# Kernel optimization log

Hardware: AMD Instinct MI355X
Metric: run time of the kernel (lower is better)

## Reference

```python
import jax, jax.numpy as jnp
import numpy as np

B, S, D, H = 4, 1024, 2048, 16
HD = D // H
SCALE = float(np.sqrt(HD))


def setup_inputs() -> dict:
    key = jax.random.key(0)
    ks = jax.random.split(key, 11)
    std = 1.0 / np.sqrt(D)
    inp = {
        'q': jax.random.normal(ks[0], (B, S, D), jnp.float32),
        'k': jax.random.normal(ks[1], (B, S, D), jnp.float32),
        'v': jax.random.normal(ks[2], (B, S, D), jnp.float32),
        'wq_w': jax.random.uniform(ks[3], (D, D), jnp.float32, -std, std),
        'wq_b': jax.random.uniform(ks[4], (D,), jnp.float32, -std, std),
        'wk_w': jax.random.uniform(ks[5], (D, D), jnp.float32, -std, std),
        'wk_b': jax.random.uniform(ks[6], (D,), jnp.float32, -std, std),
        'wv_w': jax.random.uniform(ks[7], (D, D), jnp.float32, -std, std),
        'wv_b': jax.random.uniform(ks[8], (D,), jnp.float32, -std, std),
        'wo_w': jax.random.uniform(ks[9], (D, D), jnp.float32, -std, std),
        'wo_b': jax.random.uniform(ks[10], (D,), jnp.float32, -std, std),
    }
    return inp


def reference(q, k, v, wq_w, wq_b, wk_w, wk_b, wv_w, wv_b, wo_w, wo_b):
    # Linear projections (torch Linear: x @ W.T + b), split into heads: [B,H,S,HD]
    Q = (q @ wq_w.T + wq_b).reshape(B, S, H, HD).transpose(0, 2, 1, 3)
    K = (k @ wk_w.T + wk_b).reshape(B, S, H, HD).transpose(0, 2, 1, 3)
    V = (v @ wv_w.T + wv_b).reshape(B, S, H, HD).transpose(0, 2, 1, 3)
    # scaled dot-product attention; mask=None, dropout identity (eval)
    scores = jnp.einsum('bhqd,bhkd->bhqk', Q, K) / SCALE  # [B,H,S,S]
    attn = jax.nn.softmax(scores, axis=-1)
    context = jnp.einsum('bhqk,bhkd->bhqd', attn, V)      # [B,H,S,HD]
    context = context.transpose(0, 2, 1, 3).reshape(B, S, D)
    output = context @ wo_w.T + wo_b
    return output, attn
```

## Files before the change

kernel.cpp:

```cpp
#include <hip/hip_runtime.h>
#include <hip/hip_bf16.h>


typedef __attribute__((ext_vector_type(4)))  float f32x4;
typedef __attribute__((ext_vector_type(16))) float f32x16;
typedef __attribute__((ext_vector_type(8))) short  bf16x8;
typedef __attribute__((ext_vector_type(4))) short  short4v;
typedef __attribute__((ext_vector_type(8))) short  short8v;

__device__ __forceinline__ short f2b(float f) {
  __hip_bfloat16 h = __float2bfloat16(f);
  return __builtin_bit_cast(short, h);
}
__device__ __forceinline__ float b2f(short s) {
  __hip_bfloat16 h = __builtin_bit_cast(__hip_bfloat16, s);
  return __bfloat162float(h);
}

__global__ void cast_all(
    const float* __restrict__ q,  const float* __restrict__ k,  const float* __restrict__ v,
    const float* __restrict__ w0, const float* __restrict__ w1, const float* __restrict__ w2,
    const float* __restrict__ w3,
    __hip_bfloat16* __restrict__ qd, __hip_bfloat16* __restrict__ kd, __hip_bfloat16* __restrict__ vd,
    __hip_bfloat16* __restrict__ d0, __hip_bfloat16* __restrict__ d1, __hip_bfloat16* __restrict__ d2,
    __hip_bfloat16* __restrict__ d3)
{
  const int c0 = blockIdx.x * blockDim.x + threadIdx.x;
#pragma unroll
  for (int it = 0; it < 10; ++it) {
    int c = c0 + it * 524288;
    const float* in; __hip_bfloat16* out; size_t off;
    if (c < 3145728) {
      int seg = c >> 20; off = (size_t)(c & 1048575) * 8;
      in  = seg == 0 ? q  : (seg == 1 ? k  : v);
      out = seg == 0 ? qd : (seg == 1 ? kd : vd);
    } else {
      int c2 = c - 3145728;
      int seg = c2 >> 19; off = (size_t)(c2 & 524287) * 8;
      in  = seg == 0 ? w0 : (seg == 1 ? w1 : (seg == 2 ? w2 : w3));
      out = seg == 0 ? d0 : (seg == 1 ? d1 : (seg == 2 ? d2 : d3));
    }
    float4 a = *(const float4*)(in + off);
    float4 b = *(const float4*)(in + off + 4);
    short8v o;
    o[0] = f2b(a.x); o[1] = f2b(a.y); o[2] = f2b(a.z); o[3] = f2b(a.w);
    o[4] = f2b(b.x); o[5] = f2b(b.y); o[6] = f2b(b.z); o[7] = f2b(b.w);
    *(short8v*)(out + off) = o;
  }
}

__device__ __forceinline__ void gload_lds16(const __hip_bfloat16* g, char* l) {
  __builtin_amdgcn_global_load_lds(
      (const __attribute__((address_space(1))) unsigned int*)g,
      (__attribute__((address_space(3))) unsigned int*)l, 16, 0, 0);
}

template<bool SWAP>
__device__ __forceinline__ void gemm_core64(
    const __hip_bfloat16* ga0, const __hip_bfloat16* gb0,
    char* As, char* Bs, char* lA0, char* lB0,
    int wm, int wn, int l16, int g, f32x4 (&acc)[4][4])
{
  const int sw = (l16 & 7) << 4;
#pragma unroll 1
  for (int kt = 0; kt < 32; ++kt) {
    __syncthreads();
#pragma unroll
    for (int c = 0; c < 4; ++c) {
      gload_lds16(ga0 + c * 16384, lA0 + c * 1024);
      gload_lds16(gb0 + c * 16384, lB0 + c * 1024);
    }
    ga0 += 64; gb0 += 64;
    asm volatile("s_waitcnt vmcnt(0)" ::: "memory");
    __syncthreads();
#pragma unroll
    for (int ks = 0; ks < 2; ++ks) {
      bf16x8 a[4];
#pragma unroll
      for (int mf = 0; mf < 4; ++mf)
        a[mf] = *(const bf16x8*)(As + (wm + mf * 16 + l16) * 128 + ((ks * 64 + g * 16) ^ sw));
#pragma unroll
      for (int nf = 0; nf < 4; ++nf) {
        bf16x8 b = *(const bf16x8*)(Bs + (wn + nf * 16 + l16) * 128 + ((ks * 64 + g * 16) ^ sw));
#pragma unroll
        for (int mf = 0; mf < 4; ++mf) {
          if (SWAP)
            acc[mf][nf] = __builtin_amdgcn_mfma_f32_16x16x32_bf16(b, a[mf], acc[mf][nf], 0, 0, 0);
          else
            acc[mf][nf] = __builtin_amdgcn_mfma_f32_16x16x32_bf16(a[mf], b, acc[mf][nf], 0, 0, 0);
        }
      }
    }
  }
}

__device__ __forceinline__ const __hip_bfloat16* stage_src(
    const __hip_bfloat16* M, int base, int wid, int lane) {
  return M + (size_t)(base + wid * 32 + (lane >> 3)) * 2048
           + (((lane & 7) ^ ((lane >> 3) & 7)) * 8);
}

__global__ __launch_bounds__(256, 3) void gemm_qkv(
    const __hip_bfloat16* __restrict__ qbf, const __hip_bfloat16* __restrict__ kbf,
    const __hip_bfloat16* __restrict__ vbf,
    const __hip_bfloat16* __restrict__ wqb, const __hip_bfloat16* __restrict__ wkb,
    const __hip_bfloat16* __restrict__ wvb,
    const float* __restrict__ bq, const float* __restrict__ bk, const float* __restrict__ bv,
    __hip_bfloat16* __restrict__ Qh, __hip_bfloat16* __restrict__ Kh,
    __hip_bfloat16* __restrict__ Vt)
{
  __shared__ __align__(16) char smem[32768];
  char* As = smem;
  char* Bs = smem + 16384;

  const int z = blockIdx.z;
  const __hip_bfloat16* A  = z == 0 ? qbf : (z == 1 ? kbf : vbf);
  const __hip_bfloat16* Bt = z == 0 ? wqb : (z == 1 ? wkb : wvb);
  const float* bias        = z == 0 ? bq  : (z == 1 ? bk  : bv);
  __hip_bfloat16* C        = z == 0 ? Qh  : (z == 1 ? Kh  : Vt);

  const int tid  = threadIdx.x;
  const int lane = tid & 63, wid = tid >> 6;
  const int l16  = lane & 15, g = lane >> 4;
  const int m0 = blockIdx.y * 128, n0 = blockIdx.x * 128;
  const int wm = (wid >> 1) * 64, wn = (wid & 1) * 64;

  f32x4 acc[4][4];
#pragma unroll
  for (int i = 0; i < 4; ++i)
#pragma unroll
    for (int j = 0; j < 4; ++j) acc[i][j] = f32x4{0.f, 0.f, 0.f, 0.f};

  const __hip_bfloat16* ga0 = stage_src(A,  m0, wid, lane);
  const __hip_bfloat16* gb0 = stage_src(Bt, n0, wid, lane);
  char* lA0 = As + wid * 4096;
  char* lB0 = Bs + wid * 4096;

  if (z == 2) gemm_core64<false>(ga0, gb0, As, Bs, lA0, lB0, wm, wn, l16, g, acc);
  else        gemm_core64<true >(ga0, gb0, As, Bs, lA0, lB0, wm, wn, l16, g, acc);

  const int hh = n0 >> 7, bb = m0 >> 10, sbase = m0 & 1023;
  const int c8 = (tid & 15) * 8;
  char* Cs = smem;
  if (z != 2) {
#pragma unroll
    for (int h = 0; h < 2; ++h) {
      __syncthreads();
      if ((wid >> 1) == h) {
#pragma unroll
        for (int nf = 0; nf < 4; ++nf) {
          f32x4 bvv = *(const f32x4*)(bias + n0 + wn + nf * 16 + g * 4);
#pragma unroll
          for (int mf = 0; mf < 4; ++mf) {
            int sl = mf * 16 + l16;
            int hd = wn + nf * 16 + g * 4;
            short4v pk;
#pragma unroll
            for (int r = 0; r < 4; ++r) pk[r] = f2b(acc[mf][nf][r] + bvv[r]);
            *(short4v*)(Cs + sl * 272 + hd * 2) = pk;
          }
        }
      }
      __syncthreads();
#pragma unroll
      for (int p = 0; p < 4; ++p) {
        int rl = p * 16 + (tid >> 4);
        bf16x8 val = *(const bf16x8*)(Cs + rl * 272 + c8 * 2);
        *(bf16x8*)(C + (((size_t)bb * 16 + hh) * 1024 + sbase + h * 64 + rl) * 128 + c8) = val;
      }
    }
  } else {
#pragma unroll
    for (int h = 0; h < 2; ++h) {
      __syncthreads();
      if ((wid & 1) == h) {
#pragma unroll
        for (int nf = 0; nf < 4; ++nf) {
          float bvv = bias[n0 + wn + nf * 16 + l16];
#pragma unroll
          for (int mf = 0; mf < 4; ++mf) {
            int hdl = nf * 16 + l16;
            int s0  = wm + mf * 16 + g * 4;
            short4v pk;
#pragma unroll
            for (int r = 0; r < 4; ++r) pk[r] = f2b(acc[mf][nf][r] + bvv);
            *(short4v*)(Cs + hdl * 272 + s0 * 2) = pk;
          }
        }
      }
      __syncthreads();
#pragma unroll
      for (int p = 0; p < 4; ++p) {
        int rl = p * 16 + (tid >> 4);
        bf16x8 val = *(const bf16x8*)(Cs + rl * 272 + c8 * 2);
        *(bf16x8*)(C + (((size_t)bb * 16 + hh) * 128 + h * 64 + rl) * 1024 + sbase + c8) = val;
      }
    }
  }
}

__global__ __launch_bounds__(256, 3) void gemm_out(
    const __hip_bfloat16* __restrict__ A, const __hip_bfloat16* __restrict__ Bt,
    const float* __restrict__ bias, float* __restrict__ C)
{
  __shared__ __align__(16) char smem[32768];
  char* As = smem;
  char* Bs = smem + 16384;
  const int tid  = threadIdx.x;
  const int lane = tid & 63, wid = tid >> 6;
  const int l16  = lane & 15, g = lane >> 4;
  const int m0 = blockIdx.y * 128, n0 = blockIdx.x * 128;
  const int wm = (wid >> 1) * 64, wn = (wid & 1) * 64;

  f32x4 acc[4][4];
#pragma unroll
  for (int i = 0; i < 4; ++i)
#pragma unroll
    for (int j = 0; j < 4; ++j) acc[i][j] = f32x4{0.f, 0.f, 0.f, 0.f};

  const __hip_bfloat16* ga0 = stage_src(A,  m0, wid, lane);
  const __hip_bfloat16* gb0 = stage_src(Bt, n0, wid, lane);
  char* lA0 = As + wid * 4096;
  char* lB0 = Bs + wid * 4096;

  gemm_core64<true>(ga0, gb0, As, Bs, lA0, lB0, wm, wn, l16, g, acc);

#pragma unroll
  for (int nf = 0; nf < 4; ++nf) {
    f32x4 bv = *(const f32x4*)(bias + n0 + wn + nf * 16 + g * 4);
#pragma unroll
    for (int mf = 0; mf < 4; ++mf) {
      int m = m0 + wm + mf * 16 + l16;
      int n = n0 + wn + nf * 16 + g * 4;
      f32x4 o;
#pragma unroll
      for (int r = 0; r < 4; ++r) o[r] = acc[mf][nf][r] + bv[r];
      *(f32x4*)(C + (size_t)m * 2048 + n) = o;
    }
  }
}

__global__ __launch_bounds__(512, 4) void attn_kernel(
    const __hip_bfloat16* __restrict__ Qh,
    const __hip_bfloat16* __restrict__ Kh,
    const __hip_bfloat16* __restrict__ Vt,
    float* __restrict__ attn,
    __hip_bfloat16* __restrict__ ctx)
{
  __shared__ __align__(16) char Plds[32 * 2048];
  __shared__ __align__(16) __hip_bfloat16 cs[32 * 128];
  __shared__ float red[8 * 32];
  __shared__ float invs[32];

  const int tid = threadIdx.x, lane = tid & 63, w = tid >> 6;
  const int l16 = lane & 15, g = lane >> 4;
  const int l31 = lane & 31, kh = lane >> 5;

  const int bid = blockIdx.x;
  const int xcd = bid & 7, j = bid >> 3;
  const int bh  = xcd * 8 + (j >> 5);
  const int q0  = (j & 31) << 5;

  const __hip_bfloat16* Qp = Qh + ((size_t)bh * 1024 + q0) * 128;
  const __hip_bfloat16* Kp = Kh + (size_t)bh * 1024 * 128;
  const __hip_bfloat16* Vp = Vt + (size_t)bh * 128 * 1024;
  float* ap = attn + ((size_t)bh * 1024 + q0) * 1024;

  bf16x8 qb[8];
#pragma unroll
  for (int s = 0; s < 8; ++s)
    qb[s] = *(const bf16x8*)(Qp + (size_t)l31 * 128 + s * 16 + kh * 8);

  const float esc2 = 0.12751744f;
  float rs = 0.f;

#pragma unroll
  for (int pass = 0; pass < 4; ++pass) {
    const int keybase = pass * 256 + w * 32;
    const __hip_bfloat16* kr = Kp + (size_t)(keybase + l31) * 128 + kh * 8;
    bf16x8 kb[8];
#pragma unroll
    for (int s = 0; s < 8; ++s) kb[s] = *(const bf16x8*)(kr + s * 16);
    f32x16 acc;
#pragma unroll
    for (int i = 0; i < 16; ++i) acc[i] = 0.f;
    __builtin_amdgcn_s_setprio(1);
#pragma unroll
    for (int s = 0; s < 8; ++s)
      acc = __builtin_amdgcn_mfma_f32_32x32x16_bf16(kb[s], qb[s], acc, 0, 0, 0);
    __builtin_amdgcn_s_setprio(0);
#pragma unroll
    for (int grp = 0; grp < 4; ++grp) {
      short4v pk;
#pragma unroll
      for (int jj = 0; jj < 4; ++jj) {
        float e = exp2f(acc[grp * 4 + jj] * esc2);
        rs += e;
        pk[jj] = f2b(e);
      }
      int key0 = keybase + grp * 8 + kh * 4;
      *(short4v*)(Plds + l31 * 2048 + ((key0 * 2) ^ ((l31 & 7) << 4))) = pk;
    }
  }
  rs += __shfl_xor(rs, 32, 64);
  if (lane < 32) red[w * 32 + l31] = rs;
  __syncthreads();
  if (tid < 32) {
    float t = 0.f;
#pragma unroll
    for (int ww = 0; ww < 8; ++ww) t += red[ww * 32 + tid];
    invs[tid] = 1.0f / t;
  }
  __syncthreads();

  if (w < 4) {
    f32x4 acc2[2][2];
#pragma unroll
    for (int t = 0; t < 2; ++t)
#pragma unroll
      for (int f2 = 0; f2 < 2; ++f2) acc2[t][f2] = f32x4{0.f, 0.f, 0.f, 0.f};
    const char* pr0 = Plds + l16 * 2048;
    const char* pr1 = Plds + (16 + l16) * 2048;
    const int sw = (l16 & 7) << 4;
    const __hip_bfloat16* vr0 = Vp + (size_t)(32 * w + l16) * 1024;
    const __hip_bfloat16* vr1 = Vp + (size_t)(32 * w + 16 + l16) * 1024;
#pragma unroll 4
    for (int kt = 0; kt < 32; ++kt) {
      int cb = (kt * 64 + g * 16) ^ sw;
      bf16x8 pa0 = *(const bf16x8*)(pr0 + cb);
      bf16x8 pa1 = *(const bf16x8*)(pr1 + cb);
      bf16x8 vb0 = *(const bf16x8*)(vr0 + kt * 32 + g * 8);
      bf16x8 vb1 = *(const bf16x8*)(vr1 + kt * 32 + g * 8);
      __builtin_amdgcn_s_setprio(1);
      acc2[0][0] = __builtin_amdgcn_mfma_f32_16x16x32_bf16(pa0, vb0, acc2[0][0], 0, 0, 0);
      acc2[1][0] = __builtin_amdgcn_mfma_f32_16x16x32_bf16(pa1, vb0, acc2[1][0], 0, 0, 0);
      acc2[0][1] = __builtin_amdgcn_mfma_f32_16x16x32_bf16(pa0, vb1, acc2[0][1], 0, 0, 0);
      acc2[1][1] = __builtin_amdgcn_mfma_f32_16x16x32_bf16(pa1, vb1, acc2[1][1], 0, 0, 0);
      __builtin_amdgcn_s_setprio(0);
    }
#pragma unroll
    for (int t = 0; t < 2; ++t) {
      f32x4 iv = *(const f32x4*)(invs + t * 16 + g * 4);
#pragma unroll
      for (int f2 = 0; f2 < 2; ++f2)
#pragma unroll
        for (int r = 0; r < 4; ++r)
          cs[(t * 16 + g * 4 + r) * 128 + 32 * w + f2 * 16 + l16] =
              __float2bfloat16(acc2[t][f2][r] * iv[r]);
    }
  } else {
#pragma unroll
    for (int rr = 0; rr < 2; ++rr) {
      const int row = (w - 4) * 8 + rr * 4 + g;
      const float invr = invs[row];
      const char* rp = Plds + row * 2048;
      const int swr = (row & 7) << 4;
      float* apr = ap + (size_t)row * 1024;
#pragma unroll
      for (int it = 0; it < 16; ++it) {
        int col = it * 64 + l16 * 4;
        short4v pb = *(const short4v*)(rp + ((col * 2) ^ swr));
        f32x4 val;
#pragma unroll
        for (int r = 0; r < 4; ++r) val[r] = b2f(pb[r]) * invr;
        __builtin_nontemporal_store(val, (f32x4*)(apr + col));
      }
    }
  }
  __syncthreads();

  {
    const int row = tid >> 4, c8 = (tid & 15) * 8;
    bf16x8 val = *(const bf16x8*)(cs + row * 128 + c8);
    const int bb = bh >> 4, h = bh & 15;
    *(bf16x8*)(ctx + ((size_t)(bb * 1024 + q0 + row)) * 2048 + h * 128 + c8) = val;
  }
}

extern "C" void kernel_launch(void* const* d_in, const int* in_sizes, int n_in,
                              void* d_out, int out_size, void* d_ws, size_t ws_size,
                              hipStream_t stream) {
  const float* q    = (const float*)d_in[0];
  const float* k    = (const float*)d_in[1];
  const float* v    = (const float*)d_in[2];
  const float* wq_w = (const float*)d_in[3];
  const float* wq_b = (const float*)d_in[4];
  const float* wk_w = (const float*)d_in[5];
  const float* wk_b = (const float*)d_in[6];
  const float* wv_w = (const float*)d_in[7];
  const float* wv_b = (const float*)d_in[8];
  const float* wo_w = (const float*)d_in[9];
  const float* wo_b = (const float*)d_in[10];

  const size_t BSD = (size_t)4 * 1024 * 2048;
  const size_t DD  = (size_t)2048 * 2048;

  float* out  = (float*)d_out;
  float* attn = out + BSD;

  __hip_bfloat16* qbf = (__hip_bfloat16*)attn;
  __hip_bfloat16* kbf = qbf + BSD;
  __hip_bfloat16* vbf = kbf + BSD;

  __hip_bfloat16* wqb = (__hip_bfloat16*)d_ws;
  __hip_bfloat16* wkb = wqb + DD;
  __hip_bfloat16* wvb = wkb + DD;
  __hip_bfloat16* wob = wvb + DD;
  __hip_bfloat16* Qh  = wob + DD;
  __hip_bfloat16* Kh  = Qh + BSD;
  __hip_bfloat16* Vt  = Kh + BSD;
  __hip_bfloat16* ctx = Vt + BSD;

  cast_all<<<2048, 256, 0, stream>>>(q, k, v, wq_w, wk_w, wv_w, wo_w,
                                     qbf, kbf, vbf, wqb, wkb, wvb, wob);

  gemm_qkv<<<dim3(16, 32, 3), dim3(256), 0, stream>>>(
      qbf, kbf, vbf, wqb, wkb, wvb, wq_b, wk_b, wv_b, Qh, Kh, Vt);

  attn_kernel<<<dim3(2048), dim3(512), 0, stream>>>(Qh, Kh, Vt, attn, ctx);

  gemm_out<<<dim3(16, 32), dim3(256), 0, stream>>>(ctx, wob, wo_b, out);
}
```

Before: 332.9 us.

## Double-buffer GEMM mainloop with 256x128 tiles and 8-wave blocks

```diff
diff --git a/kernel.cpp b/kernel.cpp
--- a/kernel.cpp
+++ b/kernel.cpp
@@ -56,51 +56,79 @@
 }
 
 template<bool SWAP>
-__device__ __forceinline__ void gemm_core64(
-    const __hip_bfloat16* ga0, const __hip_bfloat16* gb0,
-    char* As, char* Bs, char* lA0, char* lB0,
-    int wm, int wn, int l16, int g, f32x4 (&acc)[4][4])
+__device__ __forceinline__ void gemm8_core(
+    const __hip_bfloat16* gA, const __hip_bfloat16* gB,
+    char* smem, int wm, int wn, int l16, int g, int tid, f32x4 (&acc)[4][4])
 {
+  char* As[2] = {smem,         smem + 32768};
+  char* Bs[2] = {smem + 65536, smem + 81920};
   const int sw = (l16 & 7) << 4;
+  const size_t R64 = (size_t)64 * 2048;
+
+#pragma unroll
+  for (int c = 0; c < 4; ++c) gload_lds16(gA + c * R64, As[0] + c * 8192 + tid * 16);
+#pragma unroll
+  for (int c = 0; c < 2; ++c) gload_lds16(gB + c * R64, Bs[0] + c * 8192 + tid * 16);
+  gA += 64; gB += 64;
+
 #pragma unroll 1
-  for (int kt = 0; kt < 32; ++kt) {
+  for (int U = 0; U < 32; ++U) {
+    const int s = U & 1;
     __syncthreads();
-#pragma unroll
-    for (int c = 0; c < 4; ++c) {
-      gload_lds16(ga0 + c * 16384, lA0 + c * 1024);
-      gload_lds16(gb0 + c * 16384, lB0 + c * 1024);
-    }
-    ga0 += 64; gb0 += 64;
-    asm volatile("s_waitcnt vmcnt(0)" ::: "memory");
-    __syncthreads();
-#pragma unroll
-    for (int ks = 0; ks < 2; ++ks) {
-      bf16x8 a[4];
-#pragma unroll
-      for (int mf = 0; mf < 4; ++mf)
-        a[mf] = *(const bf16x8*)(As + (wm + mf * 16 + l16) * 128 + ((ks * 64 + g * 16) ^ sw));
-#pragma unroll
-      for (int nf = 0; nf < 4; ++nf) {
-        bf16x8 b = *(const bf16x8*)(Bs + (wn + nf * 16 + l16) * 128 + ((ks * 64 + g * 16) ^ sw));
-#pragma unroll
-        for (int mf = 0; mf < 4; ++mf) {
-          if (SWAP)
-            acc[mf][nf] = __builtin_amdgcn_mfma_f32_16x16x32_bf16(b, a[mf], acc[mf][nf], 0, 0, 0);
-          else
-            acc[mf][nf] = __builtin_amdgcn_mfma_f32_16x16x32_bf16(a[mf], b, acc[mf][nf], 0, 0, 0);
+    const bool more = (U + 1 < 32);
+#pragma unroll
+    for (int qd = 0; qd < 4; ++qd) {
+      const int mf0 = (qd >> 1) * 2, nf0 = (qd & 1) * 2;
+      bf16x8 a[2][2], b[2][2];
+#pragma unroll
+      for (int ks = 0; ks < 2; ++ks) {
+        const int cb = (ks * 64 + g * 16) ^ sw;
+#pragma unroll
+        for (int i = 0; i < 2; ++i) {
+          a[ks][i] = *(const bf16x8*)(As[s] + (wm + (mf0 + i) * 16 + l16) * 128 + cb);
+          b[ks][i] = *(const bf16x8*)(Bs[s] + (wn + (nf0 + i) * 16 + l16) * 128 + cb);
         }
       }
-    }
-  }
-}
-
-__device__ __forceinline__ const __hip_bfloat16* stage_src(
-    const __hip_bfloat16* M, int base, int wid, int lane) {
-  return M + (size_t)(base + wid * 32 + (lane >> 3)) * 2048
-           + (((lane & 7) ^ ((lane >> 3) & 7)) * 8);
-}
-
-__global__ __launch_bounds__(256, 3) void gemm_qkv(
+      if (more) {
+        if (qd == 0) {
+          gload_lds16(gA + 0 * R64, As[s ^ 1] + 0 * 8192 + tid * 16);
+          gload_lds16(gA + 1 * R64, As[s ^ 1] + 1 * 8192 + tid * 16);
+        } else if (qd == 1) {
+          gload_lds16(gA + 2 * R64, As[s ^ 1] + 2 * 8192 + tid * 16);
+          gload_lds16(gA + 3 * R64, As[s ^ 1] + 3 * 8192 + tid * 16);
+        } else if (qd == 2) {
+          gload_lds16(gB + 0 * R64, Bs[s ^ 1] + 0 * 8192 + tid * 16);
+          gload_lds16(gB + 1 * R64, Bs[s ^ 1] + 1 * 8192 + tid * 16);
+        }
+      }
+      __builtin_amdgcn_s_barrier();
+      __builtin_amdgcn_s_setprio(1);
+#pragma unroll
+      for (int ks = 0; ks < 2; ++ks)
+#pragma unroll
+        for (int i = 0; i < 2; ++i)
+#pragma unroll
+          for (int jn = 0; jn < 2; ++jn) {
+            if (SWAP)
+              acc[mf0 + i][nf0 + jn] = __builtin_amdgcn_mfma_f32_16x16x32_bf16(
+                  b[ks][jn], a[ks][i], acc[mf0 + i][nf0 + jn], 0, 0, 0);
+            else
+              acc[mf0 + i][nf0 + jn] = __builtin_amdgcn_mfma_f32_16x16x32_bf16(
+                  a[ks][i], b[ks][jn], acc[mf0 + i][nf0 + jn], 0, 0, 0);
+          }
+      __builtin_amdgcn_s_setprio(0);
+      __builtin_amdgcn_s_barrier();
+    }
+    gA += 64; gB += 64;
+  }
+}
+
+__device__ __forceinline__ const __hip_bfloat16* stage_src8(
+    const __hip_bfloat16* M, int base, int tid) {
+  return M + (size_t)(base + (tid >> 3)) * 2048 + (((tid & 7) ^ ((tid >> 3) & 7)) * 8);
+}
+
+__global__ __launch_bounds__(512, 1) void gemm_qkv(
     const __hip_bfloat16* __restrict__ qbf, const __hip_bfloat16* __restrict__ kbf,
     const __hip_bfloat16* __restrict__ vbf,
     const __hip_bfloat16* __restrict__ wqb, const __hip_bfloat16* __restrict__ wkb,
@@ -109,9 +137,7 @@
     __hip_bfloat16* __restrict__ Qh, __hip_bfloat16* __restrict__ Kh,
     __hip_bfloat16* __restrict__ Vt)
 {
-  __shared__ __align__(16) char smem[32768];
-  char* As = smem;
-  char* Bs = smem + 16384;
+  __shared__ __align__(16) char smem[98304];
 
   const int z = blockIdx.z;
   const __hip_bfloat16* A  = z == 0 ? qbf : (z == 1 ? kbf : vbf);
@@ -120,10 +146,10 @@
   __hip_bfloat16* C        = z == 0 ? Qh  : (z == 1 ? Kh  : Vt);
 
   const int tid  = threadIdx.x;
-  const int lane = tid & 63, wid = tid >> 6;
+  const int lane = tid & 63, w = tid >> 6;
   const int l16  = lane & 15, g = lane >> 4;
-  const int m0 = blockIdx.y * 128, n0 = blockIdx.x * 128;
-  const int wm = (wid >> 1) * 64, wn = (wid & 1) * 64;
+  const int m0 = blockIdx.y * 256, n0 = blockIdx.x * 128;
+  const int wm = (w >> 1) * 64, wn = (w & 1) * 64;
 
   f32x4 acc[4][4];
 #pragma unroll
@@ -131,86 +157,72 @@
 #pragma unroll
     for (int j = 0; j < 4; ++j) acc[i][j] = f32x4{0.f, 0.f, 0.f, 0.f};
 
-  const __hip_bfloat16* ga0 = stage_src(A,  m0, wid, lane);
-  const __hip_bfloat16* gb0 = stage_src(Bt, n0, wid, lane);
-  char* lA0 = As + wid * 4096;
-  char* lB0 = Bs + wid * 4096;
-
-  if (z == 2) gemm_core64<false>(ga0, gb0, As, Bs, lA0, lB0, wm, wn, l16, g, acc);
-  else        gemm_core64<true >(ga0, gb0, As, Bs, lA0, lB0, wm, wn, l16, g, acc);
-
+  const __hip_bfloat16* gA = stage_src8(A,  m0, tid);
+  const __hip_bfloat16* gB = stage_src8(Bt, n0, tid);
+
+  if (z == 2) gemm8_core<false>(gA, gB, smem, wm, wn, l16, g, tid, acc);
+  else        gemm8_core<true >(gA, gB, smem, wm, wn, l16, g, tid, acc);
+
+  __syncthreads();
   const int hh = n0 >> 7, bb = m0 >> 10, sbase = m0 & 1023;
-  const int c8 = (tid & 15) * 8;
   char* Cs = smem;
   if (z != 2) {
 #pragma unroll
-    for (int h = 0; h < 2; ++h) {
-      __syncthreads();
-      if ((wid >> 1) == h) {
-#pragma unroll
-        for (int nf = 0; nf < 4; ++nf) {
-          f32x4 bvv = *(const f32x4*)(bias + n0 + wn + nf * 16 + g * 4);
-#pragma unroll
-          for (int mf = 0; mf < 4; ++mf) {
-            int sl = mf * 16 + l16;
-            int hd = wn + nf * 16 + g * 4;
-            short4v pk;
-#pragma unroll
-            for (int r = 0; r < 4; ++r) pk[r] = f2b(acc[mf][nf][r] + bvv[r]);
-            *(short4v*)(Cs + sl * 272 + hd * 2) = pk;
-          }
-        }
-      }
-      __syncthreads();
-#pragma unroll
-      for (int p = 0; p < 4; ++p) {
-        int rl = p * 16 + (tid >> 4);
-        bf16x8 val = *(const bf16x8*)(Cs + rl * 272 + c8 * 2);
-        *(bf16x8*)(C + (((size_t)bb * 16 + hh) * 1024 + sbase + h * 64 + rl) * 128 + c8) = val;
-      }
+    for (int nf = 0; nf < 4; ++nf) {
+      f32x4 bvv = *(const f32x4*)(bias + n0 + wn + nf * 16 + g * 4);
+#pragma unroll
+      for (int mf = 0; mf < 4; ++mf) {
+        int sl = wm + mf * 16 + l16;
+        int hd = wn + nf * 16 + g * 4;
+        short4v pk;
+#pragma unroll
+        for (int r = 0; r < 4; ++r) pk[r] = f2b(acc[mf][nf][r] + bvv[r]);
+        *(short4v*)(Cs + sl * 272 + hd * 2) = pk;
+      }
+    }
+    __syncthreads();
+    const int c8 = (tid & 15) * 8;
+#pragma unroll
+    for (int p = 0; p < 8; ++p) {
+      int row = p * 32 + (tid >> 4);
+      bf16x8 val = *(const bf16x8*)(Cs + row * 272 + c8 * 2);
+      *(bf16x8*)(C + (((size_t)bb * 16 + hh) * 1024 + sbase + row) * 128 + c8) = val;
     }
   } else {
 #pragma unroll
-    for (int h = 0; h < 2; ++h) {
-      __syncthreads();
-      if ((wid & 1) == h) {
-#pragma unroll
-        for (int nf = 0; nf < 4; ++nf) {
-          float bvv = bias[n0 + wn + nf * 16 + l16];
-#pragma unroll
-          for (int mf = 0; mf < 4; ++mf) {
-            int hdl = nf * 16 + l16;
-            int s0  = wm + mf * 16 + g * 4;
-            short4v pk;
-#pragma unroll
-            for (int r = 0; r < 4; ++r) pk[r] = f2b(acc[mf][nf][r] + bvv);
-            *(short4v*)(Cs + hdl * 272 + s0 * 2) = pk;
-          }
-        }
-      }
-      __syncthreads();
-#pragma unroll
-      for (int p = 0; p < 4; ++p) {
-        int rl = p * 16 + (tid >> 4);
-        bf16x8 val = *(const bf16x8*)(Cs + rl * 272 + c8 * 2);
-        *(bf16x8*)(C + (((size_t)bb * 16 + hh) * 128 + h * 64 + rl) * 1024 + sbase + c8) = val;
-      }
-    }
-  }
-}
-
-__global__ __launch_bounds__(256, 3) void gemm_out(
+    for (int nf = 0; nf < 4; ++nf) {
+      float bvv = bias[n0 + wn + nf * 16 + l16];
+#pragma unroll
+      for (int mf = 0; mf < 4; ++mf) {
+        int hd = wn + nf * 16 + l16;
+        int sl = wm + mf * 16 + g * 4;
+        short4v pk;
+#pragma unroll
+        for (int r = 0; r < 4; ++r) pk[r] = f2b(acc[mf][nf][r] + bvv);
+        *(short4v*)(Cs + hd * 528 + sl * 2) = pk;
+      }
+    }
+    __syncthreads();
+    const int sc = (tid & 31) * 8;
+#pragma unroll
+    for (int p = 0; p < 8; ++p) {
+      int hd = p * 16 + (tid >> 5);
+      bf16x8 val = *(const bf16x8*)(Cs + hd * 528 + sc * 2);
+      *(bf16x8*)(C + (((size_t)bb * 16 + hh) * 128 + hd) * 1024 + sbase + sc) = val;
+    }
+  }
+}
+
+__global__ __launch_bounds__(512, 1) void gemm_out(
     const __hip_bfloat16* __restrict__ A, const __hip_bfloat16* __restrict__ Bt,
     const float* __restrict__ bias, float* __restrict__ C)
 {
-  __shared__ __align__(16) char smem[32768];
-  char* As = smem;
-  char* Bs = smem + 16384;
+  __shared__ __align__(16) char smem[98304];
   const int tid  = threadIdx.x;
-  const int lane = tid & 63, wid = tid >> 6;
+  const int lane = tid & 63, w = tid >> 6;
   const int l16  = lane & 15, g = lane >> 4;
-  const int m0 = blockIdx.y * 128, n0 = blockIdx.x * 128;
-  const int wm = (wid >> 1) * 64, wn = (wid & 1) * 64;
+  const int m0 = blockIdx.y * 256, n0 = blockIdx.x * 128;
+  const int wm = (w >> 1) * 64, wn = (w & 1) * 64;
 
   f32x4 acc[4][4];
 #pragma unroll
@@ -218,12 +230,10 @@
 #pragma unroll
     for (int j = 0; j < 4; ++j) acc[i][j] = f32x4{0.f, 0.f, 0.f, 0.f};
 
-  const __hip_bfloat16* ga0 = stage_src(A,  m0, wid, lane);
-  const __hip_bfloat16* gb0 = stage_src(Bt, n0, wid, lane);
-  char* lA0 = As + wid * 4096;
-  char* lB0 = Bs + wid * 4096;
-
-  gemm_core64<true>(ga0, gb0, As, Bs, lA0, lB0, wm, wn, l16, g, acc);
+  const __hip_bfloat16* gA = stage_src8(A,  m0, tid);
+  const __hip_bfloat16* gB = stage_src8(Bt, n0, tid);
+
+  gemm8_core<true>(gA, gB, smem, wm, wn, l16, g, tid, acc);
 
 #pragma unroll
   for (int nf = 0; nf < 4; ++nf) {
@@ -414,10 +424,10 @@
   cast_all<<<2048, 256, 0, stream>>>(q, k, v, wq_w, wk_w, wv_w, wo_w,
                                      qbf, kbf, vbf, wqb, wkb, wvb, wob);
 
-  gemm_qkv<<<dim3(16, 32, 3), dim3(256), 0, stream>>>(
+  gemm_qkv<<<dim3(16, 16, 3), dim3(512), 0, stream>>>(
       qbf, kbf, vbf, wqb, wkb, wvb, wq_b, wk_b, wv_b, Qh, Kh, Vt);
 
   attn_kernel<<<dim3(2048), dim3(512), 0, stream>>>(Qh, Kh, Vt, attn, ctx);
 
-  gemm_out<<<dim3(16, 32), dim3(256), 0, stream>>>(ctx, wob, wo_b, out);
-}
+  gemm_out<<<dim3(16, 16), dim3(512), 0, stream>>>(ctx, wob, wo_b, out);
+}
```

New measurement: 632.0 us. +89.8%, slower.
